# Performance work log

Hardware: AMD Instinct MI355X
Metric: run time of the kernel (lower is better)

## Reference

```python
import jax, jax.numpy as jnp
import numpy as np

N = 1_000_000   # total nodes
B = 1024        # number of graphs
H = 64          # node feature dim / LSTM hidden
STEPS = 5       # Set2Set processing steps
PROJ = 128      # projection_dim


def setup_inputs() -> dict:
    key = jax.random.key(0)
    ks = jax.random.split(key, 12)
    x = jax.random.normal(ks[0], (N, H), dtype=jnp.float32)
    batch = jnp.sort(jax.random.randint(ks[1], (N,), 0, B)).astype(jnp.int64)
    s = 1.0 / np.sqrt(H)
    # torch.nn.LSTM(input_size=2H, hidden_size=H), gate order i,f,g,o
    W_ih = jax.random.uniform(ks[2], (4 * H, 2 * H), minval=-s, maxval=s, dtype=jnp.float32)
    W_hh = jax.random.uniform(ks[3], (4 * H, H), minval=-s, maxval=s, dtype=jnp.float32)
    b_ih = jax.random.uniform(ks[4], (4 * H,), minval=-s, maxval=s, dtype=jnp.float32)
    b_hh = jax.random.uniform(ks[5], (4 * H,), minval=-s, maxval=s, dtype=jnp.float32)
    s1 = 1.0 / np.sqrt(2 * H)
    W1 = jax.random.uniform(ks[6], (256, 2 * H), minval=-s1, maxval=s1, dtype=jnp.float32)
    b1 = jax.random.uniform(ks[7], (256,), minval=-s1, maxval=s1, dtype=jnp.float32)
    s2 = 1.0 / np.sqrt(256)
    W2 = jax.random.uniform(ks[8], (PROJ, 256), minval=-s2, maxval=s2, dtype=jnp.float32)
    b2 = jax.random.uniform(ks[9], (PROJ,), minval=-s2, maxval=s2, dtype=jnp.float32)
    return {"x": x, "batch": batch, "W_ih": W_ih, "W_hh": W_hh, "b_ih": b_ih,
            "b_hh": b_hh, "W1": W1, "b1": b1, "W2": W2, "b2": b2}


def _set2set(x, batch, W_ih, W_hh, b_ih, b_hh):
    q_star = jnp.zeros((B, 2 * H), x.dtype)
    h = jnp.zeros((B, H), x.dtype)
    c = jnp.zeros((B, H), x.dtype)
    for _ in range(STEPS):
        gates = q_star @ W_ih.T + b_ih + h @ W_hh.T + b_hh
        i, f, g, o = jnp.split(gates, 4, axis=-1)
        i = jax.nn.sigmoid(i); f = jax.nn.sigmoid(f)
        g = jnp.tanh(g); o = jax.nn.sigmoid(o)
        c = f * c + i * g
        h = o * jnp.tanh(c)
        q = h  # [B, H]
        # segment-wise attention over ragged node sets
        e = jnp.sum(x * q[batch], axis=-1)                         # [N]
        emax = jax.ops.segment_max(e, batch, num_segments=B)       # [B]
        a = jnp.exp(e - emax[batch])
        denom = jax.ops.segment_sum(a, batch, num_segments=B)
        a = a / jnp.maximum(denom, 1e-16)[batch]
        r = jax.ops.segment_sum(a[:, None] * x, batch, num_segments=B)  # [B, H]
        q_star = jnp.concatenate([q, r], axis=-1)
    return q_star


def reference(x, batch, W_ih, W_hh, b_ih, b_hh, W1, b1, W2, b2):
    out = _set2set(x, batch, W_ih, W_hh, b_ih, b_hh)   # [B, 2H]
    out = out @ W1.T + b1                               # [B, 256]
    out = jax.nn.relu(out) @ W2.T + b2                  # [B, PROJ]
    return out
```

## Files before the change

### kernel.cpp

```cpp
#include <hip/hip_runtime.h>
#include <float.h>
#include <math.h>

#define NB 1024
#define HD 64
#define NSTEPS 5
#define PROJ_D 128

__device__ __forceinline__ float sigmoidf_(float x) {
    return 1.0f / (1.0f + __expf(-x));
}

__global__ void init_state_kernel(float* __restrict__ q_star,
                                  float* __restrict__ h,
                                  float* __restrict__ c) {
    int i = blockIdx.x * blockDim.x + threadIdx.x;
    if (i < NB * 2 * HD) q_star[i] = 0.0f;
    if (i < NB * HD) { h[i] = 0.0f; c[i] = 0.0f; }
}

__global__ void seg_bounds_kernel(const int* __restrict__ batch,
                                  int* __restrict__ seg_start, int n) {
    int i = blockIdx.x * blockDim.x + threadIdx.x;
    if (i >= n) return;
    int b = batch[i];
    if (i == 0) {
        for (int j = 0; j <= b; ++j) seg_start[j] = 0;
    } else {
        int pb = batch[i - 1];
        for (int j = pb + 1; j <= b; ++j) seg_start[j] = i;
    }
    if (i == n - 1) {
        for (int j = b + 1; j <= NB; ++j) seg_start[j] = n;
    }
}

__global__ void lstm_kernel(const float* __restrict__ W_ih,
                            const float* __restrict__ W_hh,
                            const float* __restrict__ b_ih,
                            const float* __restrict__ b_hh,
                            float* __restrict__ q_star,
                            float* __restrict__ h,
                            float* __restrict__ c) {
    const int G = 8;
    int g0 = blockIdx.x * G;
    __shared__ float s_qs[G][128];
    __shared__ float s_h[G][64];
    __shared__ float s_gates[G][256];
    int tid = threadIdx.x;

    for (int idx = tid; idx < G * 128; idx += 256) {
        int g = idx >> 7, k = idx & 127;
        s_qs[g][k] = q_star[(g0 + g) * 128 + k];
    }
    for (int idx = tid; idx < G * 64; idx += 256) {
        int g = idx >> 6, k = idx & 63;
        s_h[g][k] = h[(g0 + g) * 64 + k];
    }
    __syncthreads();

    int j = tid;
    float acc[G];
    float bias = b_ih[j] + b_hh[j];
#pragma unroll
    for (int g = 0; g < G; ++g) acc[g] = bias;
    const float* wih = W_ih + j * 128;
    for (int k = 0; k < 128; ++k) {
        float w = wih[k];
#pragma unroll
        for (int g = 0; g < G; ++g) acc[g] = fmaf(w, s_qs[g][k], acc[g]);
    }
    const float* whh = W_hh + j * 64;
    for (int k = 0; k < 64; ++k) {
        float w = whh[k];
#pragma unroll
        for (int g = 0; g < G; ++g) acc[g] = fmaf(w, s_h[g][k], acc[g]);
    }
#pragma unroll
    for (int g = 0; g < G; ++g) s_gates[g][j] = acc[g];
    __syncthreads();

    for (int idx = tid; idx < G * 64; idx += 256) {
        int g = idx >> 6, jj = idx & 63;
        int gb = g0 + g;
        float ig = sigmoidf_(s_gates[g][jj]);
        float fg = sigmoidf_(s_gates[g][jj + 64]);
        float gg = tanhf(s_gates[g][jj + 128]);
        float og = sigmoidf_(s_gates[g][jj + 192]);
        float cn = fmaf(fg, c[gb * 64 + jj], ig * gg);
        float hn = og * tanhf(cn);
        c[gb * 64 + jj] = cn;
        h[gb * 64 + jj] = hn;
        q_star[gb * 128 + jj] = hn;
    }
}

__global__ __launch_bounds__(256) void attn_kernel(const float* __restrict__ x,
                                                   const int* __restrict__ seg_start,
                                                   float* __restrict__ q_star) {
    int b = blockIdx.x;
    int s = seg_start[b], e = seg_start[b + 1];
    int tid = threadIdx.x;
    int lane = tid & 63;
    int wave = tid >> 6;
    int quad = lane >> 2;
    int p = lane & 3;

    float q[16];
    const float* qsrc = q_star + b * 128 + p * 16;
#pragma unroll
    for (int k = 0; k < 16; ++k) q[k] = qsrc[k];

    float m = -FLT_MAX, sum = 0.0f;
    float r[16];
#pragma unroll
    for (int k = 0; k < 16; ++k) r[k] = 0.0f;

    for (int base = s; base < e; base += 64) {
        int node = base + wave * 16 + quad;
        bool valid = node < e;
        float xv[16];
        if (valid) {
            const float4* xp = (const float4*)(x + (size_t)node * 64 + p * 16);
            float4 a0 = xp[0], a1 = xp[1], a2 = xp[2], a3 = xp[3];
            xv[0] = a0.x; xv[1] = a0.y; xv[2] = a0.z; xv[3] = a0.w;
            xv[4] = a1.x; xv[5] = a1.y; xv[6] = a1.z; xv[7] = a1.w;
            xv[8] = a2.x; xv[9] = a2.y; xv[10] = a2.z; xv[11] = a2.w;
            xv[12] = a3.x; xv[13] = a3.y; xv[14] = a3.z; xv[15] = a3.w;
        } else {
#pragma unroll
            for (int k = 0; k < 16; ++k) xv[k] = 0.0f;
        }
        float dot = 0.0f;
#pragma unroll
        for (int k = 0; k < 16; ++k) dot = fmaf(xv[k], q[k], dot);
        dot += __shfl_xor(dot, 1);
        dot += __shfl_xor(dot, 2);
        float eeff = valid ? dot : -FLT_MAX;
        float nm = fmaxf(m, eeff);
        float scale = __expf(m - nm);
        float w = valid ? __expf(eeff - nm) : 0.0f;
        sum = fmaf(sum, scale, w);
#pragma unroll
        for (int k = 0; k < 16; ++k) r[k] = fmaf(r[k], scale, w * xv[k]);
        m = nm;
    }

#pragma unroll
    for (int off = 4; off < 64; off <<= 1) {
        float om = __shfl_xor(m, off);
        float os = __shfl_xor(sum, off);
        float orr[16];
#pragma unroll
        for (int k = 0; k < 16; ++k) orr[k] = __shfl_xor(r[k], off);
        float nm = fmaxf(m, om);
        float sc1 = __expf(m - nm);
        float sc2 = __expf(om - nm);
        sum = sum * sc1 + os * sc2;
#pragma unroll
        for (int k = 0; k < 16; ++k) r[k] = r[k] * sc1 + orr[k] * sc2;
        m = nm;
    }

    __shared__ float lm[4], ls[4], lr[4][64];
    if (lane < 4) {
        if (lane == 0) { lm[wave] = m; ls[wave] = sum; }
#pragma unroll
        for (int k = 0; k < 16; ++k) lr[wave][lane * 16 + k] = r[k];
    }
    __syncthreads();
    if (tid < 64) {
        float M = fmaxf(fmaxf(lm[0], lm[1]), fmaxf(lm[2], lm[3]));
        float w0 = __expf(lm[0] - M), w1 = __expf(lm[1] - M);
        float w2 = __expf(lm[2] - M), w3 = __expf(lm[3] - M);
        float S = ls[0] * w0 + ls[1] * w1 + ls[2] * w2 + ls[3] * w3;
        float rf = lr[0][tid] * w0 + lr[1][tid] * w1 + lr[2][tid] * w2 + lr[3][tid] * w3;
        float denom = fmaxf(S, 1e-16f);
        q_star[b * 128 + 64 + tid] = rf / denom;
    }
}

__global__ void mlp_kernel(const float* __restrict__ q_star,
                           const float* __restrict__ W1,
                           const float* __restrict__ b1,
                           const float* __restrict__ W2,
                           const float* __restrict__ b2,
                           float* __restrict__ out) {
    int b = blockIdx.x;
    __shared__ float qs[128];
    __shared__ float hid[256];
    int tid = threadIdx.x;
    if (tid < 128) qs[tid] = q_star[b * 128 + tid];
    __syncthreads();
    float acc = b1[tid];
    const float* w = W1 + tid * 128;
    for (int k = 0; k < 128; ++k) acc = fmaf(w[k], qs[k], acc);
    hid[tid] = fmaxf(acc, 0.0f);
    __syncthreads();
    if (tid < 128) {
        float acc2 = b2[tid];
        const float* w2 = W2 + tid * 256;
        for (int k = 0; k < 256; ++k) acc2 = fmaf(w2[k], hid[k], acc2);
        out[b * 128 + tid] = acc2;
    }
}

extern "C" void kernel_launch(void* const* d_in, const int* in_sizes, int n_in,
                              void* d_out, int out_size, void* d_ws, size_t ws_size,
                              hipStream_t stream) {
    const float* x    = (const float*)d_in[0];
    const int*   batch= (const int*)d_in[1];
    const float* W_ih = (const float*)d_in[2];
    const float* W_hh = (const float*)d_in[3];
    const float* b_ih = (const float*)d_in[4];
    const float* b_hh = (const float*)d_in[5];
    const float* W1   = (const float*)d_in[6];
    const float* b1   = (const float*)d_in[7];
    const float* W2   = (const float*)d_in[8];
    const float* b2   = (const float*)d_in[9];
    float* out = (float*)d_out;
    const int N = in_sizes[1];

    float* q_star = (float*)d_ws;
    float* h      = q_star + NB * 128;
    float* c      = h + NB * 64;
    int*   seg    = (int*)(c + NB * 64);

    init_state_kernel<<<(NB * 2 * HD + 255) / 256, 256, 0, stream>>>(q_star, h, c);
    seg_bounds_kernel<<<(N + 255) / 256, 256, 0, stream>>>(batch, seg, N);

    for (int step = 0; step < NSTEPS; ++step) {
        lstm_kernel<<<NB / 8, 256, 0, stream>>>(W_ih, W_hh, b_ih, b_hh, q_star, h, c);
        attn_kernel<<<NB, 256, 0, stream>>>(x, seg, q_star);
    }
    mlp_kernel<<<NB, 256, 0, stream>>>(q_star, W1, b1, W2, b2, out);
}
```

Baseline: 632.7 us.

## Split each graph's attention across four blocks and merge partials in consumers

The attention kernel now launches four blocks per graph, each computing a partial online softmax (max, sum, weighted sum) over a quarter of the graph's nodes. The LSTM and MLP kernels merge these partials when they load their inputs. The q_star buffer and the init kernel are removed, and the first LSTM step skips its matmul because the state is zero. The goal is more blocks in flight for the memory-bound x scans; in exchange the merge work is repeated in the consumer kernels. Weight loads are also vectorised to float4, and out-of-range node loads are clamped so that load is no longer branchy.

```diff
diff --git a/kernel.cpp b/kernel.cpp
--- a/kernel.cpp
+++ b/kernel.cpp
@@ -5,18 +5,10 @@
 #define NB 1024
 #define HD 64
 #define NSTEPS 5
-#define PROJ_D 128
+#define SPLIT 4
 
 __device__ __forceinline__ float sigmoidf_(float x) {
     return 1.0f / (1.0f + __expf(-x));
-}
-
-__global__ void init_state_kernel(float* __restrict__ q_star,
-                                  float* __restrict__ h,
-                                  float* __restrict__ c) {
-    int i = blockIdx.x * blockDim.x + threadIdx.x;
-    if (i < NB * 2 * HD) q_star[i] = 0.0f;
-    if (i < NB * HD) { h[i] = 0.0f; c[i] = 0.0f; }
 }
 
 __global__ void seg_bounds_kernel(const int* __restrict__ batch,
@@ -39,42 +31,73 @@
                             const float* __restrict__ W_hh,
                             const float* __restrict__ b_ih,
                             const float* __restrict__ b_hh,
-                            float* __restrict__ q_star,
+                            const float* __restrict__ pm,
+                            const float* __restrict__ ps,
+                            const float* __restrict__ pr,
                             float* __restrict__ h,
-                            float* __restrict__ c) {
+                            float* __restrict__ c,
+                            int first) {
     const int G = 8;
     int g0 = blockIdx.x * G;
     __shared__ float s_qs[G][128];
-    __shared__ float s_h[G][64];
     __shared__ float s_gates[G][256];
     int tid = threadIdx.x;
 
-    for (int idx = tid; idx < G * 128; idx += 256) {
-        int g = idx >> 7, k = idx & 127;
-        s_qs[g][k] = q_star[(g0 + g) * 128 + k];
-    }
-    for (int idx = tid; idx < G * 64; idx += 256) {
-        int g = idx >> 6, k = idx & 63;
-        s_h[g][k] = h[(g0 + g) * 64 + k];
-    }
-    __syncthreads();
+    if (!first) {
+        for (int idx = tid; idx < G * 64; idx += 256) {
+            int g = idx >> 6, k = idx & 63;
+            s_qs[g][k] = h[(g0 + g) * 64 + k];
+        }
+        for (int idx = tid; idx < G * 64; idx += 256) {
+            int g = idx >> 6, k = idx & 63;
+            int b = g0 + g;
+            float m0 = pm[b * SPLIT + 0], m1 = pm[b * SPLIT + 1];
+            float m2 = pm[b * SPLIT + 2], m3 = pm[b * SPLIT + 3];
+            float M = fmaxf(fmaxf(m0, m1), fmaxf(m2, m3));
+            float w0 = __expf(m0 - M), w1 = __expf(m1 - M);
+            float w2 = __expf(m2 - M), w3 = __expf(m3 - M);
+            float S = ps[b * SPLIT + 0] * w0 + ps[b * SPLIT + 1] * w1
+                    + ps[b * SPLIT + 2] * w2 + ps[b * SPLIT + 3] * w3;
+            float rf = pr[(b * SPLIT + 0) * 64 + k] * w0
+                     + pr[(b * SPLIT + 1) * 64 + k] * w1
+                     + pr[(b * SPLIT + 2) * 64 + k] * w2
+                     + pr[(b * SPLIT + 3) * 64 + k] * w3;
+            s_qs[g][64 + k] = rf / fmaxf(S, 1e-16f);
+        }
+        __syncthreads();
+    }
 
     int j = tid;
     float acc[G];
     float bias = b_ih[j] + b_hh[j];
 #pragma unroll
     for (int g = 0; g < G; ++g) acc[g] = bias;
-    const float* wih = W_ih + j * 128;
-    for (int k = 0; k < 128; ++k) {
-        float w = wih[k];
-#pragma unroll
-        for (int g = 0; g < G; ++g) acc[g] = fmaf(w, s_qs[g][k], acc[g]);
-    }
-    const float* whh = W_hh + j * 64;
-    for (int k = 0; k < 64; ++k) {
-        float w = whh[k];
-#pragma unroll
-        for (int g = 0; g < G; ++g) acc[g] = fmaf(w, s_h[g][k], acc[g]);
+
+    if (!first) {
+        const float4* wih = (const float4*)(W_ih + j * 128);
+#pragma unroll 4
+        for (int k4 = 0; k4 < 32; ++k4) {
+            float4 w = wih[k4];
+#pragma unroll
+            for (int g = 0; g < G; ++g) {
+                acc[g] = fmaf(w.x, s_qs[g][k4 * 4 + 0], acc[g]);
+                acc[g] = fmaf(w.y, s_qs[g][k4 * 4 + 1], acc[g]);
+                acc[g] = fmaf(w.z, s_qs[g][k4 * 4 + 2], acc[g]);
+                acc[g] = fmaf(w.w, s_qs[g][k4 * 4 + 3], acc[g]);
+            }
+        }
+        const float4* whh = (const float4*)(W_hh + j * 64);
+#pragma unroll 4
+        for (int k4 = 0; k4 < 16; ++k4) {
+            float4 w = whh[k4];
+#pragma unroll
+            for (int g = 0; g < G; ++g) {
+                acc[g] = fmaf(w.x, s_qs[g][k4 * 4 + 0], acc[g]);
+                acc[g] = fmaf(w.y, s_qs[g][k4 * 4 + 1], acc[g]);
+                acc[g] = fmaf(w.z, s_qs[g][k4 * 4 + 2], acc[g]);
+                acc[g] = fmaf(w.w, s_qs[g][k4 * 4 + 3], acc[g]);
+            }
+        }
     }
 #pragma unroll
     for (int g = 0; g < G; ++g) s_gates[g][j] = acc[g];
@@ -87,19 +110,28 @@
         float fg = sigmoidf_(s_gates[g][jj + 64]);
         float gg = tanhf(s_gates[g][jj + 128]);
         float og = sigmoidf_(s_gates[g][jj + 192]);
-        float cn = fmaf(fg, c[gb * 64 + jj], ig * gg);
+        float cprev = first ? 0.0f : c[gb * 64 + jj];
+        float cn = fmaf(fg, cprev, ig * gg);
         float hn = og * tanhf(cn);
         c[gb * 64 + jj] = cn;
         h[gb * 64 + jj] = hn;
-        q_star[gb * 128 + jj] = hn;
     }
 }
 
 __global__ __launch_bounds__(256) void attn_kernel(const float* __restrict__ x,
                                                    const int* __restrict__ seg_start,
-                                                   float* __restrict__ q_star) {
-    int b = blockIdx.x;
-    int s = seg_start[b], e = seg_start[b + 1];
+                                                   const float* __restrict__ h,
+                                                   float* __restrict__ pm,
+                                                   float* __restrict__ ps,
+                                                   float* __restrict__ pr) {
+    int bs = blockIdx.x;
+    int b = bs >> 2;
+    int slice = bs & (SPLIT - 1);
+    int s0 = seg_start[b], e0 = seg_start[b + 1];
+    int len = e0 - s0;
+    int s = s0 + (int)(((long long)len * slice) >> 2);
+    int e = s0 + (int)(((long long)len * (slice + 1)) >> 2);
+
     int tid = threadIdx.x;
     int lane = tid & 63;
     int wave = tid >> 6;
@@ -107,7 +139,7 @@
     int p = lane & 3;
 
     float q[16];
-    const float* qsrc = q_star + b * 128 + p * 16;
+    const float* qsrc = h + b * 64 + p * 16;
 #pragma unroll
     for (int k = 0; k < 16; ++k) q[k] = qsrc[k];
 
@@ -119,23 +151,21 @@
     for (int base = s; base < e; base += 64) {
         int node = base + wave * 16 + quad;
         bool valid = node < e;
+        int nc = valid ? node : (e - 1);
+        const float4* xp = (const float4*)(x + (size_t)nc * 64 + p * 16);
+        float4 a0 = xp[0], a1 = xp[1], a2 = xp[2], a3 = xp[3];
         float xv[16];
-        if (valid) {
-            const float4* xp = (const float4*)(x + (size_t)node * 64 + p * 16);
-            float4 a0 = xp[0], a1 = xp[1], a2 = xp[2], a3 = xp[3];
-            xv[0] = a0.x; xv[1] = a0.y; xv[2] = a0.z; xv[3] = a0.w;
-            xv[4] = a1.x; xv[5] = a1.y; xv[6] = a1.z; xv[7] = a1.w;
-            xv[8] = a2.x; xv[9] = a2.y; xv[10] = a2.z; xv[11] = a2.w;
-            xv[12] = a3.x; xv[13] = a3.y; xv[14] = a3.z; xv[15] = a3.w;
-        } else {
-#pragma unroll
-            for (int k = 0; k < 16; ++k) xv[k] = 0.0f;
-        }
+        xv[0] = a0.x; xv[1] = a0.y; xv[2] = a0.z; xv[3] = a0.w;
+        xv[4] = a1.x; xv[5] = a1.y; xv[6] = a1.z; xv[7] = a1.w;
+        xv[8] = a2.x; xv[9] = a2.y; xv[10] = a2.z; xv[11] = a2.w;
+        xv[12] = a3.x; xv[13] = a3.y; xv[14] = a3.z; xv[15] = a3.w;
+
         float dot = 0.0f;
 #pragma unroll
         for (int k = 0; k < 16; ++k) dot = fmaf(xv[k], q[k], dot);
         dot += __shfl_xor(dot, 1);
         dot += __shfl_xor(dot, 2);
+
         float eeff = valid ? dot : -FLT_MAX;
         float nm = fmaxf(m, eeff);
         float scale = __expf(m - nm);
@@ -175,12 +205,15 @@
         float w2 = __expf(lm[2] - M), w3 = __expf(lm[3] - M);
         float S = ls[0] * w0 + ls[1] * w1 + ls[2] * w2 + ls[3] * w3;
         float rf = lr[0][tid] * w0 + lr[1][tid] * w1 + lr[2][tid] * w2 + lr[3][tid] * w3;
-        float denom = fmaxf(S, 1e-16f);
-        q_star[b * 128 + 64 + tid] = rf / denom;
-    }
-}
-
-__global__ void mlp_kernel(const float* __restrict__ q_star,
+        if (tid == 0) { pm[bs] = M; ps[bs] = S; }
+        pr[bs * 64 + tid] = rf;
+    }
+}
+
+__global__ void mlp_kernel(const float* __restrict__ h,
+                           const float* __restrict__ pm,
+                           const float* __restrict__ ps,
+                           const float* __restrict__ pr,
                            const float* __restrict__ W1,
                            const float* __restrict__ b1,
                            const float* __restrict__ W2,
@@ -190,17 +223,47 @@
     __shared__ float qs[128];
     __shared__ float hid[256];
     int tid = threadIdx.x;
-    if (tid < 128) qs[tid] = q_star[b * 128 + tid];
+    if (tid < 64) {
+        qs[tid] = h[b * 64 + tid];
+    } else if (tid < 128) {
+        int k = tid - 64;
+        float m0 = pm[b * SPLIT + 0], m1 = pm[b * SPLIT + 1];
+        float m2 = pm[b * SPLIT + 2], m3 = pm[b * SPLIT + 3];
+        float M = fmaxf(fmaxf(m0, m1), fmaxf(m2, m3));
+        float w0 = __expf(m0 - M), w1 = __expf(m1 - M);
+        float w2 = __expf(m2 - M), w3 = __expf(m3 - M);
+        float S = ps[b * SPLIT + 0] * w0 + ps[b * SPLIT + 1] * w1
+                + ps[b * SPLIT + 2] * w2 + ps[b * SPLIT + 3] * w3;
+        float rf = pr[(b * SPLIT + 0) * 64 + k] * w0
+                 + pr[(b * SPLIT + 1) * 64 + k] * w1
+                 + pr[(b * SPLIT + 2) * 64 + k] * w2
+                 + pr[(b * SPLIT + 3) * 64 + k] * w3;
+        qs[tid] = rf / fmaxf(S, 1e-16f);
+    }
     __syncthreads();
     float acc = b1[tid];
-    const float* w = W1 + tid * 128;
-    for (int k = 0; k < 128; ++k) acc = fmaf(w[k], qs[k], acc);
+    const float4* w = (const float4*)(W1 + tid * 128);
+#pragma unroll 4
+    for (int k4 = 0; k4 < 32; ++k4) {
+        float4 ww = w[k4];
+        acc = fmaf(ww.x, qs[k4 * 4 + 0], acc);
+        acc = fmaf(ww.y, qs[k4 * 4 + 1], acc);
+        acc = fmaf(ww.z, qs[k4 * 4 + 2], acc);
+        acc = fmaf(ww.w, qs[k4 * 4 + 3], acc);
+    }
     hid[tid] = fmaxf(acc, 0.0f);
     __syncthreads();
     if (tid < 128) {
         float acc2 = b2[tid];
-        const float* w2 = W2 + tid * 256;
-        for (int k = 0; k < 256; ++k) acc2 = fmaf(w2[k], hid[k], acc2);
+        const float4* w2 = (const float4*)(W2 + tid * 256);
+#pragma unroll 4
+        for (int k4 = 0; k4 < 64; ++k4) {
+            float4 ww = w2[k4];
+            acc2 = fmaf(ww.x, hid[k4 * 4 + 0], acc2);
+            acc2 = fmaf(ww.y, hid[k4 * 4 + 1], acc2);
+            acc2 = fmaf(ww.z, hid[k4 * 4 + 2], acc2);
+            acc2 = fmaf(ww.w, hid[k4 * 4 + 3], acc2);
+        }
         out[b * 128 + tid] = acc2;
     }
 }
@@ -221,17 +284,19 @@
     float* out = (float*)d_out;
     const int N = in_sizes[1];
 
-    float* q_star = (float*)d_ws;
-    float* h      = q_star + NB * 128;
-    float* c      = h + NB * 64;
-    int*   seg    = (int*)(c + NB * 64);
-
-    init_state_kernel<<<(NB * 2 * HD + 255) / 256, 256, 0, stream>>>(q_star, h, c);
+    float* h   = (float*)d_ws;
+    float* c   = h + NB * 64;
+    int*   seg = (int*)(c + NB * 64);
+    float* pm  = (float*)(seg + NB + 8);
+    float* ps  = pm + NB * SPLIT;
+    float* pr  = ps + NB * SPLIT;
+
     seg_bounds_kernel<<<(N + 255) / 256, 256, 0, stream>>>(batch, seg, N);
 
     for (int step = 0; step < NSTEPS; ++step) {
-        lstm_kernel<<<NB / 8, 256, 0, stream>>>(W_ih, W_hh, b_ih, b_hh, q_star, h, c);
-        attn_kernel<<<NB, 256, 0, stream>>>(x, seg, q_star);
-    }
-    mlp_kernel<<<NB, 256, 0, stream>>>(q_star, W1, b1, W2, b2, out);
-}
+        lstm_kernel<<<NB / 8, 256, 0, stream>>>(W_ih, W_hh, b_ih, b_hh,
+                                                pm, ps, pr, h, c, step == 0 ? 1 : 0);
+        attn_kernel<<<NB * SPLIT, 256, 0, stream>>>(x, seg, h, pm, ps, pr);
+    }
+    mlp_kernel<<<NB, 256, 0, stream>>>(h, pm, ps, pr, W1, b1, W2, b2, out);
+}
```

Result: faster. 618.9 us (-2.2%).
